# Kernel tuning notes

Hardware: AMD Instinct MI355X
Metric: run time of the kernel (lower is better)

The kernel has to match this reference:

```python
import jax, jax.numpy as jnp
import numpy as np

D_MODEL = 1024
N_HEADS = 16
HEAD_DIM = D_MODEL // N_HEADS


def setup_inputs() -> dict:
    key = jax.random.key(0)
    ks = jax.random.split(key, 5)
    B, T = 4, 2048
    x = jax.random.normal(ks[0], (B, T, D_MODEL), dtype=jnp.float32)
    s = 1.0 / np.sqrt(D_MODEL)
    W_qkv = jax.random.normal(ks[1], (D_MODEL, 3 * D_MODEL), dtype=jnp.float32) * s
    b_qkv = jnp.zeros((3 * D_MODEL,), dtype=jnp.float32)
    W_out = jax.random.normal(ks[2], (D_MODEL, D_MODEL), dtype=jnp.float32) * s
    b_out = jnp.zeros((D_MODEL,), dtype=jnp.float32)
    return {"x": x, "W_qkv": W_qkv, "b_qkv": b_qkv, "W_out": W_out, "b_out": b_out}


def reference(x, W_qkv, b_qkv, W_out, b_out):
    B, T, C = x.shape
    qkv = x @ W_qkv + b_qkv                      # [B,T,3C]
    q, k, v = jnp.split(qkv, 3, axis=-1)
    # [B,T,H,Dh] -> [B,H,T,Dh]
    q = q.reshape(B, T, N_HEADS, HEAD_DIM).transpose(0, 2, 1, 3)
    k = k.reshape(B, T, N_HEADS, HEAD_DIM).transpose(0, 2, 1, 3)
    v = v.reshape(B, T, N_HEADS, HEAD_DIM).transpose(0, 2, 1, 3)
    scale = HEAD_DIM ** -0.5
    attn = jnp.einsum('bhqd,bhkd->bhqk', q, k) * scale
    causal = jnp.triu(jnp.ones((T, T), dtype=bool), k=1)
    attn = jnp.where(causal, -jnp.inf, attn)
    attn = jax.nn.softmax(attn, axis=-1)
    out = jnp.einsum('bhqk,bhkd->bhqd', attn, v)
    out = out.transpose(0, 2, 1, 3).reshape(B, T, C)
    return out @ W_out + b_out
```

## Files before the change

### kernel.cpp

```cpp
#include <hip/hip_runtime.h>
#include <hip/hip_bf16.h>


typedef unsigned short u16;
typedef __attribute__((ext_vector_type(8))) short short8;
typedef __attribute__((ext_vector_type(4))) short short4v;
typedef __attribute__((ext_vector_type(4))) float f32x4;

#define N_HEADS 16
#define HEAD_DIM 64
#define TSEQ 2048
#define BATCH 4
#define MROWS (BATCH * TSEQ)
#define N3 3072

__device__ __forceinline__ void cp16(const u16* g, u16* l) {
  __builtin_amdgcn_global_load_lds((const __attribute__((address_space(1))) void*)g,
                                   (__attribute__((address_space(3))) void*)l, 16, 0, 0);
}

__device__ __forceinline__ f32x4 mfma16(short8 a, short8 b, f32x4 c) {
  return __builtin_amdgcn_mfma_f32_16x16x32_bf16(a, b, c, 0, 0, 0);
}

__device__ __forceinline__ u16 f2b(float f) {
  __hip_bfloat16 h = __float2bfloat16(f);
  return *reinterpret_cast<u16*>(&h);
}

#define PREP_CVT_BLOCKS 8192
#define PREP_WQKV_BLOCKS (96 * 32)
#define PREP_WOUT_BLOCKS (32 * 32)
#define PREP_TOTAL (PREP_CVT_BLOCKS + PREP_WQKV_BLOCKS + PREP_WOUT_BLOCKS)

__device__ __forceinline__ void transpose_tile(const float* __restrict__ src,
                                               u16* __restrict__ dst,
                                               int R, int Cn, int c0, int r0,
                                               float (*tile)[33]) {
  const int tx = threadIdx.x & 31, ty = threadIdx.x >> 5;
  for (int i = ty; i < 32; i += 8)
    tile[i][tx] = src[(size_t)(r0 + i) * Cn + c0 + tx];
  __syncthreads();
  for (int i = ty; i < 32; i += 8)
    dst[(size_t)(c0 + i) * R + r0 + tx] = f2b(tile[tx][i]);
}

__global__ __launch_bounds__(256) void prep_kernel(
    const float* __restrict__ x, u16* __restrict__ xb,
    const float* __restrict__ Wqkv, u16* __restrict__ wqkv_t,
    const float* __restrict__ Wout, u16* __restrict__ wout_t) {
  __shared__ float tile[32][33];
  const int bx = blockIdx.x;
  if (bx < PREP_CVT_BLOCKS) {
    int i = bx * 256 + threadIdx.x;
    float4 v = *(const float4*)(x + (size_t)i * 4);
    u16* d = xb + (size_t)i * 4;
    d[0] = f2b(v.x); d[1] = f2b(v.y); d[2] = f2b(v.z); d[3] = f2b(v.w);
  } else if (bx < PREP_CVT_BLOCKS + PREP_WQKV_BLOCKS) {
    int b2 = bx - PREP_CVT_BLOCKS;
    int c0 = (b2 % 96) * 32, r0 = (b2 / 96) * 32;
    transpose_tile(Wqkv, wqkv_t, 1024, N3, c0, r0, tile);
  } else {
    int b3 = bx - PREP_CVT_BLOCKS - PREP_WQKV_BLOCKS;
    int c0 = (b3 % 32) * 32, r0 = (b3 / 32) * 32;
    transpose_tile(Wout, wout_t, 1024, 1024, c0, r0, tile);
  }
}

__device__ __forceinline__ void gemm128_sync(const u16* __restrict__ A,
                                             const u16* __restrict__ Bt,
                                             int m0, int n0,
                                             u16* Asm, u16* Bsm,
                                             f32x4 acc[4][4]) {
  const int tid = threadIdx.x;
  const int w = tid >> 6;
  const int lane = tid & 63;
  const int quad = lane >> 4;
  const int l16 = lane & 15;
  const int wm = (w >> 1) * 64;
  const int wn = (w & 1) * 64;

#pragma unroll
  for (int i = 0; i < 4; ++i)
#pragma unroll
    for (int j = 0; j < 4; ++j) acc[i][j] = (f32x4){0.f, 0.f, 0.f, 0.f};

  for (int k0 = 0; k0 < 1024; k0 += 32) {
    __syncthreads();
#pragma unroll
    for (int p = 0; p < 2; ++p) {
      int s = p * 256 + tid;
      int row = s >> 2;
      int c4 = (s & 3) ^ ((row >> 1) & 3);
      cp16(A + (size_t)(m0 + row) * 1024 + k0 + c4 * 8,
           Asm + (size_t)(p * 256 + w * 64) * 8);
      cp16(Bt + (size_t)(n0 + row) * 1024 + k0 + c4 * 8,
           Bsm + (size_t)(p * 256 + w * 64) * 8);
    }
    __syncthreads();

    short8 a[4], b[4];
#pragma unroll
    for (int i = 0; i < 4; ++i) {
      int row = wm + i * 16 + l16;
      int c4 = quad ^ ((row >> 1) & 3);
      a[i] = *(const short8*)(Asm + row * 32 + c4 * 8);
    }
#pragma unroll
    for (int j = 0; j < 4; ++j) {
      int row = wn + j * 16 + l16;
      int c4 = quad ^ ((row >> 1) & 3);
      b[j] = *(const short8*)(Bsm + row * 32 + c4 * 8);
    }
#pragma unroll
    for (int i = 0; i < 4; ++i)
#pragma unroll
      for (int j = 0; j < 4; ++j)
        acc[i][j] = mfma16(a[i], b[j], acc[i][j]);
  }
}

__device__ __forceinline__ void gemm128_pipe(const u16* __restrict__ A,
                                             const u16* __restrict__ Bt,
                                             int m0, int n0,
                                             u16* Asm, u16* Bsm,
                                             f32x4 acc[4][4]) {
  const int tid = threadIdx.x;
  const int w = tid >> 6;
  const int lane = tid & 63;
  const int quad = lane >> 4;
  const int l16 = lane & 15;
  const int wm = (w >> 1) * 64;
  const int wn = (w & 1) * 64;

#pragma unroll
  for (int i = 0; i < 4; ++i)
#pragma unroll
    for (int j = 0; j < 4; ++j) acc[i][j] = (f32x4){0.f, 0.f, 0.f, 0.f};

#define STG128(k0_, b_)                                                     \
  do {                                                                      \
    _Pragma("unroll")                                                       \
    for (int p = 0; p < 2; ++p) {                                           \
      int s = p * 256 + tid;                                                \
      int row = s >> 2;                                                     \
      int c4 = (s & 3) ^ ((row >> 1) & 3);                                  \
      cp16(A + (size_t)(m0 + row) * 1024 + (k0_) + c4 * 8,                  \
           Asm + (size_t)(b_) * 4096 + (p * 256 + w * 64) * 8);             \
      cp16(Bt + (size_t)(n0 + row) * 1024 + (k0_) + c4 * 8,                 \
           Bsm + (size_t)(b_) * 4096 + (p * 256 + w * 64) * 8);             \
    }                                                                       \
  } while (0)

  STG128(0, 0);
  STG128(32, 1);
  asm volatile("s_waitcnt vmcnt(4)" ::: "memory");
  asm volatile("s_barrier" ::: "memory");

  for (int kt = 0; kt < 32; ++kt) {
    const u16* Ab = Asm + (kt & 1) * 4096;
    const u16* Bb = Bsm + (kt & 1) * 4096;
    short8 a[4], b[4];
#pragma unroll
    for (int i = 0; i < 4; ++i) {
      int row = wm + i * 16 + l16;
      int c4 = quad ^ ((row >> 1) & 3);
      a[i] = *(const short8*)(Ab + row * 32 + c4 * 8);
    }
#pragma unroll
    for (int j = 0; j < 4; ++j) {
      int row = wn + j * 16 + l16;
      int c4 = quad ^ ((row >> 1) & 3);
      b[j] = *(const short8*)(Bb + row * 32 + c4 * 8);
    }
#pragma unroll
    for (int i = 0; i < 4; ++i)
#pragma unroll
      for (int j = 0; j < 4; ++j)
        acc[i][j] = mfma16(a[i], b[j], acc[i][j]);

    asm volatile("s_barrier" ::: "memory");
    if (kt + 2 < 32) {
      STG128((kt + 2) * 32, kt & 1);
      asm volatile("s_waitcnt vmcnt(4)" ::: "memory");
    } else if (kt + 1 < 32) {
      asm volatile("s_waitcnt vmcnt(0)" ::: "memory");
    }
    asm volatile("s_barrier" ::: "memory");
  }
#undef STG128
}

__global__ __launch_bounds__(256) void gemm_qkv_kernel(
    const u16* __restrict__ x, const u16* __restrict__ Wt,
    const float* __restrict__ bias,
    u16* __restrict__ qb, u16* __restrict__ kb, u16* __restrict__ vtb) {
  __shared__ __align__(16) u16 Asm[128 * 32];
  __shared__ __align__(16) u16 Bsm[128 * 32];
  f32x4 acc[4][4];
  const int m0 = blockIdx.y * 128;
  const int n0 = blockIdx.x * 128;
  gemm128_sync(x, Wt, m0, n0, Asm, Bsm, acc);

  const int tid = threadIdx.x;
  const int w = tid >> 6, lane = tid & 63, quad = lane >> 4, l16 = lane & 15;
  const int wm = (w >> 1) * 64, wn = (w & 1) * 64;
#pragma unroll
  for (int j = 0; j < 4; ++j) {
    int col = n0 + wn + j * 16 + l16;
    float bv = bias[col];
    int which = col >> 10;
    int rem = col & 1023;
    int h = rem >> 6, d = rem & 63;
#pragma unroll
    for (int i = 0; i < 4; ++i) {
      int m4 = m0 + wm + i * 16 + quad * 4;
      int b_ = m4 >> 11, t4 = m4 & 2047;
      int bh = b_ * N_HEADS + h;
      if (which == 2) {
        short4v pk;
#pragma unroll
        for (int r = 0; r < 4; ++r) pk[r] = (short)f2b(acc[i][j][r] + bv);
        *(short4v*)(vtb + ((size_t)((bh << 6) + d)) * TSEQ + t4) = pk;
      } else {
        u16* dst = (which == 0) ? qb : kb;
#pragma unroll
        for (int r = 0; r < 4; ++r)
          dst[((size_t)(bh * TSEQ + t4 + r) << 6) + d] = f2b(acc[i][j][r] + bv);
      }
    }
  }
}

__global__ __launch_bounds__(256, 5) void attn_kernel(const u16* __restrict__ qb,
                                                      const u16* __restrict__ kb,
                                                      const u16* __restrict__ vtb,
                                                      u16* __restrict__ ob) {
  const int flat = blockIdx.y * 16 + blockIdx.x;
  const int swz = (flat & 7) * 128 + (flat >> 3);
  const int bh = swz >> 4;
  const int qt = 15 - (swz & 15);
  __shared__ __align__(16) u16 Ksm[2][4096];
  __shared__ __align__(16) u16 Vsm[2][4096];
  const int tid = threadIdx.x;
  const int w = tid >> 6, lane = tid & 63, quad = lane >> 4, l16 = lane & 15;
  const int qbase = qt * 128;

  short8 qf[2][2];
#pragma unroll
  for (int mi = 0; mi < 2; ++mi) {
    const u16* qr = qb + ((size_t)(bh * TSEQ + qbase + mi * 64 + w * 16 + l16)) * 64;
    qf[mi][0] = *(const short8*)(qr + quad * 8);
    qf[mi][1] = *(const short8*)(qr + 32 + quad * 8);
  }

  f32x4 o[2][4];
  float lp[2] = {0.f, 0.f};
#pragma unroll
  for (int mi = 0; mi < 2; ++mi)
#pragma unroll
    for (int j = 0; j < 4; ++j) o[mi][j] = (f32x4){0.f, 0.f, 0.f, 0.f};
  const float cexp = 0.18033688011112042f;
  const float M = 10.0f;

  const u16* kb_bh = kb + (size_t)bh * TSEQ * 64;
  const u16* vt_bh = vtb + (size_t)bh * 64 * TSEQ;
  const int nk = 2 * qt + 2;

#define STAGE(kt_, b_)                                                        \
  do {                                                                        \
    const u16* kbase_ = kb_bh + (size_t)((kt_) * 64) * 64;                    \
    const u16* vbase_ = vt_bh + (kt_) * 64;                                   \
    _Pragma("unroll")                                                         \
    for (int p = 0; p < 2; ++p) {                                             \
      int s_ = p * 256 + tid;                                                 \
      int row_ = s_ >> 3;                                                     \
      int c8_ = (s_ & 7) ^ (row_ & 7);                                        \
      int krow_ = (row_ & 0x23) | ((row_ & 0x0C) << 1) | ((row_ & 0x10) >> 2);\
      cp16(kbase_ + krow_ * 64 + c8_ * 8, &Ksm[b_][(p * 256 + w * 64) * 8]);  \
      cp16(vbase_ + (size_t)row_ * TSEQ + c8_ * 8,                            \
           &Vsm[b_][(p * 256 + w * 64) * 8]);                                 \
    }                                                                         \
  } while (0)

  STAGE(0, 0);

  for (int kt = 0; kt < nk; ++kt) {
    asm volatile("s_barrier" ::: "memory");
    if (kt + 1 < nk) {
      STAGE(kt + 1, (kt + 1) & 1);
      asm volatile("s_waitcnt vmcnt(4)" ::: "memory");
    } else {
      asm volatile("s_waitcnt vmcnt(0)" ::: "memory");
    }
    asm volatile("s_barrier" ::: "memory");

    const u16* Kb = Ksm[kt & 1];
    const u16* Vb = Vsm[kt & 1];

    __builtin_amdgcn_s_setprio(1);
#pragma unroll
    for (int mi = 0; mi < 2; ++mi) {
      const int qmin = qbase + mi * 64 + w * 16;
      if (kt * 64 > qmin + 15) continue;
      const int qlane = qmin + l16;

      f32x4 s[4];
#pragma unroll
      for (int j = 0; j < 4; ++j) {
        int row = j * 16 + l16;
        int ca = quad ^ (row & 7);
        int cb = (4 + quad) ^ (row & 7);
        short8 k0 = *(const short8*)(Kb + row * 64 + ca * 8);
        short8 k1 = *(const short8*)(Kb + row * 64 + cb * 8);
        f32x4 z = (f32x4){0.f, 0.f, 0.f, 0.f};
        z = mfma16(k0, qf[mi][0], z);
        z = mfma16(k1, qf[mi][1], z);
        s[j] = z;
      }
      if (kt * 64 + 63 > qmin) {
#pragma unroll
        for (int j = 0; j < 4; ++j) {
#pragma unroll
          for (int r = 0; r < 4; ++r) {
            int kabs = kt * 64 + ((j >> 1) << 5) + (quad << 3) + ((j & 1) << 2) + r;
            if (kabs > qlane) s[j][r] = -1e30f;
          }
        }
      }
      short8 ap0, ap1;
#pragma unroll
      for (int j = 0; j < 4; ++j) {
#pragma unroll
        for (int r = 0; r < 4; ++r) {
          float p_ = __builtin_amdgcn_exp2f(__builtin_fmaf(s[j][r], cexp, -M));
          lp[mi] += p_;
          u16 pb = f2b(p_);
          if (j < 2) ap0[j * 4 + r] = (short)pb;
          else       ap1[(j - 2) * 4 + r] = (short)pb;
        }
      }
#pragma unroll
      for (int j = 0; j < 4; ++j) {
        int row = j * 16 + l16;
        int ca = quad ^ (row & 7);
        int cb = (4 + quad) ^ (row & 7);
        short8 v0 = *(const short8*)(Vb + row * 64 + ca * 8);
        short8 v1 = *(const short8*)(Vb + row * 64 + cb * 8);
        o[mi][j] = mfma16(ap0, v0, o[mi][j]);
        o[mi][j] = mfma16(ap1, v1, o[mi][j]);
      }
    }
    __builtin_amdgcn_s_setprio(0);
  }
#undef STAGE

#pragma unroll
  for (int mi = 0; mi < 2; ++mi) {
    lp[mi] += __shfl_xor(lp[mi], 16);
    lp[mi] += __shfl_xor(lp[mi], 32);
  }
  const int b_ = bh >> 4, h = bh & 15;
#pragma unroll
  for (int mi = 0; mi < 2; ++mi) {
    float dn[4];
#pragma unroll
    for (int r = 0; r < 4; ++r)
      dn[r] = __shfl(lp[mi], (lane & 48) + quad * 4 + r);
#pragma unroll
    for (int j = 0; j < 4; ++j)
#pragma unroll
      for (int r = 0; r < 4; ++r) {
        int t = qbase + mi * 64 + w * 16 + quad * 4 + r;
        int d = j * 16 + l16;
        ob[((size_t)(b_ * TSEQ + t)) * 1024 + h * 64 + d] =
            f2b(o[mi][j][r] / dn[r]);
      }
  }
}

__global__ __launch_bounds__(256) void gemm_out_kernel(
    const u16* __restrict__ attn, const u16* __restrict__ Wt,
    const float* __restrict__ bias, float* __restrict__ out) {
  __shared__ __align__(16) u16 Asm[2 * 4096];
  __shared__ __align__(16) u16 Bsm[2 * 4096];
  f32x4 acc[4][4];
  const int flat = blockIdx.y * 8 + blockIdx.x;
  const int swz = (flat & 7) * 64 + (flat >> 3);
  const int m0 = (swz >> 3) * 128;
  const int n0 = (swz & 7) * 128;
  gemm128_pipe(attn, Wt, m0, n0, Asm, Bsm, acc);

  const int tid = threadIdx.x;
  const int w = tid >> 6, lane = tid & 63, quad = lane >> 4, l16 = lane & 15;
  const int wm = (w >> 1) * 64, wn = (w & 1) * 64;
#pragma unroll
  for (int j = 0; j < 4; ++j) {
    int col = n0 + wn + j * 16 + l16;
    float bv = bias[col];
#pragma unroll
    for (int i = 0; i < 4; ++i)
#pragma unroll
      for (int r = 0; r < 4; ++r) {
        int m = m0 + wm + i * 16 + quad * 4 + r;
        out[(size_t)m * 1024 + col] = acc[i][j][r] + bv;
      }
  }
}

extern "C" void kernel_launch(void* const* d_in, const int* in_sizes, int n_in,
                              void* d_out, int out_size, void* d_ws, size_t ws_size,
                              hipStream_t stream) {
  const float* x    = (const float*)d_in[0];
  const float* Wqkv = (const float*)d_in[1];
  const float* bqkv = (const float*)d_in[2];
  const float* Wout = (const float*)d_in[3];
  const float* bout = (const float*)d_in[4];
  float* out = (float*)d_out;

  u16* ws = (u16*)d_ws;
  u16* xb     = ws;
  u16* wqkv_t = xb + (size_t)MROWS * 1024;
  u16* wout_t = wqkv_t + (size_t)N3 * 1024;
  u16* qbuf   = wout_t + (size_t)1024 * 1024;
  u16* kbuf   = qbuf + (size_t)MROWS * 1024;
  u16* vtbuf  = kbuf + (size_t)MROWS * 1024;
  u16* obuf   = vtbuf + (size_t)MROWS * 1024;
  (void)ws_size; (void)n_in; (void)in_sizes; (void)out_size;

  prep_kernel<<<PREP_TOTAL, 256, 0, stream>>>(x, xb, Wqkv, wqkv_t, Wout, wout_t);
  gemm_qkv_kernel<<<dim3(N3 / 128, MROWS / 128), 256, 0, stream>>>(xb, wqkv_t, bqkv, qbuf, kbuf, vtbuf);
  attn_kernel<<<dim3(TSEQ / 128, BATCH * N_HEADS), 256, 0, stream>>>(qbuf, kbuf, vtbuf, obuf);
  gemm_out_kernel<<<dim3(8, 64), 256, 0, stream>>>(obuf, wout_t, bout, out);
}
```

Before: 278.6 us.

## Split attention query tile across 8 waves instead of 4 with two row-blocks each

```diff
diff --git a/kernel.cpp b/kernel.cpp
--- a/kernel.cpp
+++ b/kernel.cpp
@@ -232,7 +232,7 @@
   }
 }
 
-__global__ __launch_bounds__(256, 5) void attn_kernel(const u16* __restrict__ qb,
+__global__ __launch_bounds__(512, 8) void attn_kernel(const u16* __restrict__ qb,
                                                       const u16* __restrict__ kb,
                                                       const u16* __restrict__ vtb,
                                                       u16* __restrict__ ob) {
@@ -245,21 +245,19 @@
   const int tid = threadIdx.x;
   const int w = tid >> 6, lane = tid & 63, quad = lane >> 4, l16 = lane & 15;
   const int qbase = qt * 128;
-
-  short8 qf[2][2];
-#pragma unroll
-  for (int mi = 0; mi < 2; ++mi) {
-    const u16* qr = qb + ((size_t)(bh * TSEQ + qbase + mi * 64 + w * 16 + l16)) * 64;
-    qf[mi][0] = *(const short8*)(qr + quad * 8);
-    qf[mi][1] = *(const short8*)(qr + 32 + quad * 8);
-  }
-
-  f32x4 o[2][4];
-  float lp[2] = {0.f, 0.f};
-#pragma unroll
-  for (int mi = 0; mi < 2; ++mi)
-#pragma unroll
-    for (int j = 0; j < 4; ++j) o[mi][j] = (f32x4){0.f, 0.f, 0.f, 0.f};
+  const int qmin = qbase + w * 16;
+
+  short8 qf0, qf1;
+  {
+    const u16* qr = qb + ((size_t)(bh * TSEQ + qmin + l16)) * 64;
+    qf0 = *(const short8*)(qr + quad * 8);
+    qf1 = *(const short8*)(qr + 32 + quad * 8);
+  }
+
+  f32x4 o[4];
+  float lp = 0.f;
+#pragma unroll
+  for (int j = 0; j < 4; ++j) o[j] = (f32x4){0.f, 0.f, 0.f, 0.f};
   const float cexp = 0.18033688011112042f;
   const float M = 10.0f;
 
@@ -271,16 +269,11 @@
   do {                                                                        \
     const u16* kbase_ = kb_bh + (size_t)((kt_) * 64) * 64;                    \
     const u16* vbase_ = vt_bh + (kt_) * 64;                                   \
-    _Pragma("unroll")                                                         \
-    for (int p = 0; p < 2; ++p) {                                             \
-      int s_ = p * 256 + tid;                                                 \
-      int row_ = s_ >> 3;                                                     \
-      int c8_ = (s_ & 7) ^ (row_ & 7);                                        \
-      int krow_ = (row_ & 0x23) | ((row_ & 0x0C) << 1) | ((row_ & 0x10) >> 2);\
-      cp16(kbase_ + krow_ * 64 + c8_ * 8, &Ksm[b_][(p * 256 + w * 64) * 8]);  \
-      cp16(vbase_ + (size_t)row_ * TSEQ + c8_ * 8,                            \
-           &Vsm[b_][(p * 256 + w * 64) * 8]);                                 \
-    }                                                                         \
+    int row_ = tid >> 3;                                                      \
+    int c8_ = (tid & 7) ^ (row_ & 7);                                         \
+    int krow_ = (row_ & 0x23) | ((row_ & 0x0C) << 1) | ((row_ & 0x10) >> 2);  \
+    cp16(kbase_ + krow_ * 64 + c8_ * 8, &Ksm[b_][w * 512]);                   \
+    cp16(vbase_ + (size_t)row_ * TSEQ + c8_ * 8, &Vsm[b_][w * 512]);          \
   } while (0)
 
   STAGE(0, 0);
@@ -289,7 +282,7 @@
     asm volatile("s_barrier" ::: "memory");
     if (kt + 1 < nk) {
       STAGE(kt + 1, (kt + 1) & 1);
-      asm volatile("s_waitcnt vmcnt(4)" ::: "memory");
+      asm volatile("s_waitcnt vmcnt(2)" ::: "memory");
     } else {
       asm volatile("s_waitcnt vmcnt(0)" ::: "memory");
     }
@@ -298,11 +291,8 @@
     const u16* Kb = Ksm[kt & 1];
     const u16* Vb = Vsm[kt & 1];
 
-    __builtin_amdgcn_s_setprio(1);
-#pragma unroll
-    for (int mi = 0; mi < 2; ++mi) {
-      const int qmin = qbase + mi * 64 + w * 16;
-      if (kt * 64 > qmin + 15) continue;
+    if (kt * 64 <= qmin + 15) {
+      __builtin_amdgcn_s_setprio(1);
       const int qlane = qmin + l16;
 
       f32x4 s[4];
@@ -314,8 +304,8 @@
         short8 k0 = *(const short8*)(Kb + row * 64 + ca * 8);
         short8 k1 = *(const short8*)(Kb + row * 64 + cb * 8);
         f32x4 z = (f32x4){0.f, 0.f, 0.f, 0.f};
-        z = mfma16(k0, qf[mi][0], z);
-        z = mfma16(k1, qf[mi][1], z);
+        z = mfma16(k0, qf0, z);
+        z = mfma16(k1, qf1, z);
         s[j] = z;
       }
       if (kt * 64 + 63 > qmin) {
@@ -334,7 +324,7 @@
 #pragma unroll
         for (int r = 0; r < 4; ++r) {
           float p_ = __builtin_amdgcn_exp2f(__builtin_fmaf(s[j][r], cexp, -M));
-          lp[mi] += p_;
+          lp += p_;
           u16 pb = f2b(p_);
           if (j < 2) ap0[j * 4 + r] = (short)pb;
           else       ap1[(j - 2) * 4 + r] = (short)pb;
@@ -347,36 +337,30 @@
         int cb = (4 + quad) ^ (row & 7);
         short8 v0 = *(const short8*)(Vb + row * 64 + ca * 8);
         short8 v1 = *(const short8*)(Vb + row * 64 + cb * 8);
-        o[mi][j] = mfma16(ap0, v0, o[mi][j]);
-        o[mi][j] = mfma16(ap1, v1, o[mi][j]);
-      }
-    }
-    __builtin_amdgcn_s_setprio(0);
+        o[j] = mfma16(ap0, v0, o[j]);
+        o[j] = mfma16(ap1, v1, o[j]);
+      }
+      __builtin_amdgcn_s_setprio(0);
+    }
   }
 #undef STAGE
 
-#pragma unroll
-  for (int mi = 0; mi < 2; ++mi) {
-    lp[mi] += __shfl_xor(lp[mi], 16);
-    lp[mi] += __shfl_xor(lp[mi], 32);
-  }
+  lp += __shfl_xor(lp, 16);
+  lp += __shfl_xor(lp, 32);
   const int b_ = bh >> 4, h = bh & 15;
-#pragma unroll
-  for (int mi = 0; mi < 2; ++mi) {
-    float dn[4];
-#pragma unroll
-    for (int r = 0; r < 4; ++r)
-      dn[r] = __shfl(lp[mi], (lane & 48) + quad * 4 + r);
-#pragma unroll
-    for (int j = 0; j < 4; ++j)
-#pragma unroll
-      for (int r = 0; r < 4; ++r) {
-        int t = qbase + mi * 64 + w * 16 + quad * 4 + r;
-        int d = j * 16 + l16;
-        ob[((size_t)(b_ * TSEQ + t)) * 1024 + h * 64 + d] =
-            f2b(o[mi][j][r] / dn[r]);
-      }
-  }
+  float dn[4];
+#pragma unroll
+  for (int r = 0; r < 4; ++r)
+    dn[r] = __shfl(lp, (lane & 48) + quad * 4 + r);
+#pragma unroll
+  for (int j = 0; j < 4; ++j)
+#pragma unroll
+    for (int r = 0; r < 4; ++r) {
+      int t = qmin + quad * 4 + r;
+      int d = j * 16 + l16;
+      ob[((size_t)(b_ * TSEQ + t)) * 1024 + h * 64 + d] =
+          f2b(o[j][r] / dn[r]);
+    }
 }
 
 __global__ __launch_bounds__(256) void gemm_out_kernel(
@@ -430,6 +414,6 @@
 
   prep_kernel<<<PREP_TOTAL, 256, 0, stream>>>(x, xb, Wqkv, wqkv_t, Wout, wout_t);
   gemm_qkv_kernel<<<dim3(N3 / 128, MROWS / 128), 256, 0, stream>>>(xb, wqkv_t, bqkv, qbuf, kbuf, vtbuf);
-  attn_kernel<<<dim3(TSEQ / 128, BATCH * N_HEADS), 256, 0, stream>>>(qbuf, kbuf, vtbuf, obuf);
+  attn_kernel<<<dim3(TSEQ / 128, BATCH * N_HEADS), 512, 0, stream>>>(qbuf, kbuf, vtbuf, obuf);
   gemm_out_kernel<<<dim3(8, 64), 256, 0, stream>>>(obuf, wout_t, bout, out);
 }
```

New measurement: 252.2 us. 9.5% less time.
